# Kernel optimization log

Hardware: AMD Instinct MI355X
Metric: run time of the kernel (lower is better)

Reference implementation:

```python
import jax, jax.numpy as jnp
import numpy as np

TEMPERATURE = 1.0
WEIGHT = 1.0


def _transitivity_sum(rel):
    """rel: [N, N] relation probabilities for one (batch, relation) slice.
    Computes sum_{a,b,c} relu(rel[a,b] - rel[a,c] * rel[b,c]) via a scan over c
    (outer product of column c), keeping memory at O(N^2) instead of O(N^3)."""
    def step(acc, col):  # col = rel[:, c], shape [N]
        viol = jax.nn.relu(rel - col[:, None] * col[None, :])  # [N, N]
        return acc + jnp.sum(viol), None
    acc, _ = jax.lax.scan(step, jnp.zeros((), rel.dtype), rel.T)
    return acc


def setup_inputs() -> dict:
    key = jax.random.key(0)
    B, N, R = 2, 512, 4
    relation_logits = jax.random.normal(key, (B, N, N, R), dtype=jnp.float32)
    entity_masks = jnp.ones((B, N), dtype=jnp.int32)
    return {"relation_logits": relation_logits, "entity_masks": entity_masks}


def reference(relation_logits, entity_masks):
    B, N, _, R = relation_logits.shape
    probs = jax.nn.sigmoid(relation_logits / TEMPERATURE)  # [B, N, N, R]
    m = (entity_masks > 0).astype(probs.dtype)             # [B, N]
    rel = probs * m[:, :, None, None] * m[:, None, :, None]
    # flatten (batch, relation) and vmap the per-matrix cubic reduction
    rel_br = jnp.transpose(rel, (0, 3, 1, 2)).reshape(B * R, N, N)
    per = jax.vmap(_transitivity_sum)(rel_br)              # [B*R]
    # per-batch loss = sum_r / R; final = weight * mean over batch
    return WEIGHT * jnp.sum(per) / (R * B)
```

## Files before the change

kernel.cpp:

```cpp
#include <hip/hip_runtime.h>
#include <math.h>

#define N      512
#define RNUM   4
#define BNUM   2
#define NSLICE (RNUM * BNUM)
#define TILE   128
#define CT     32
#define LSTR   136
#define CSPLIT 8
#define NCOLB  16
#define SCALE  0.0625f

typedef _Float16 half2_t __attribute__((ext_vector_type(2)));

__device__ __forceinline__ unsigned int h2u(half2_t h) {
  return __builtin_bit_cast(unsigned int, h);
}
__device__ __forceinline__ half2_t u2h(unsigned int u) {
  return __builtin_bit_cast(half2_t, u);
}

__device__ __forceinline__ float sigmoidf_(float x) {
  return 1.0f / (1.0f + __expf(-x));
}

__global__ void zero_out_kernel(float* out) { out[0] = 0.0f; }

__global__ __launch_bounds__(256) void prep_f16_kernel(const float* __restrict__ logits,
                                                       const int* __restrict__ masks,
                                                       _Float16* __restrict__ P,
                                                       float* __restrict__ out) {
  if (blockIdx.x == 0 && threadIdx.x == 0) out[0] = 0.0f;
  int t = blockIdx.x * 256 + threadIdx.x;
  int b = t >> 18;
  int rem = t & (N * N - 1);
  int i = rem >> 9;
  int j = rem & (N - 1);
  float4 lg = *(const float4*)(logits + (size_t)t * 4);
  float mm = ((masks[b * N + i] > 0) && (masks[b * N + j] > 0)) ? 1.0f : 0.0f;
  size_t base = (size_t)b * RNUM * N * N + rem;
  P[base + 0 * (size_t)N * N] = (_Float16)(mm * sigmoidf_(lg.x));
  P[base + 1 * (size_t)N * N] = (_Float16)(mm * sigmoidf_(lg.y));
  P[base + 2 * (size_t)N * N] = (_Float16)(mm * sigmoidf_(lg.z));
  P[base + 3 * (size_t)N * N] = (_Float16)(mm * sigmoidf_(lg.w));
}

__global__ __launch_bounds__(256) void work_f16_kernel(const _Float16* __restrict__ P,
                                                       float* __restrict__ out) {
  __shared__ _Float16 tA[CT][LSTR];
  __shared__ _Float16 tB[CT][LSTR];
  __shared__ float wsum[4];

  const int tid = threadIdx.x;
  const int bid = blockIdx.x;

  if (bid < NCOLB) {
    const int s    = bid >> 1;
    const int half = bid & 1;
    const int c    = half * 256 + tid;
    const _Float16* col = P + (size_t)s * N * N + c;
    float sum = 0.0f;
#pragma unroll 8
    for (int a = 0; a < N; ++a) sum += (float)col[(size_t)a * N];
    float v = sum * ((float)N - sum);
    for (int off = 32; off > 0; off >>= 1) v += __shfl_down(v, off, 64);
    const int wid = tid >> 6;
    if ((tid & 63) == 0) wsum[wid] = v;
    __syncthreads();
    if (tid == 0)
      atomicAdd(out, (wsum[0] + wsum[1] + wsum[2] + wsum[3]) * SCALE);
    return;
  }

  const int m  = bid - NCOLB;
  const int bt = m & 3;
  const int at = (m >> 2) & 3;
  const int s  = (m >> 4) & 7;
  const int cz = m >> 7;
  const int a0 = at * TILE;
  const int b0 = bt * TILE;
  const int cbeg = cz * (N / CSPLIT);
  const int cend = cbeg + (N / CSPLIT);

  const int ta = tid & 15;
  const int tb = tid >> 4;

  const _Float16* Ph = P + (size_t)s * N * N;

  half2_t nrab2[8][4];
#pragma unroll
  for (int x = 0; x < 8; ++x) {
    int ga = a0 + ((x >> 2) << 6) + ta * 4 + (x & 3);
    uint2 u0 = *(const uint2*)(Ph + (size_t)ga * N + b0 + tb * 4);
    uint2 u1 = *(const uint2*)(Ph + (size_t)ga * N + b0 + 64 + tb * 4);
    nrab2[x][0] = u2h(u0.x ^ 0x80008000u);
    nrab2[x][1] = u2h(u0.y ^ 0x80008000u);
    nrab2[x][2] = u2h(u1.x ^ 0x80008000u);
    nrab2[x][3] = u2h(u1.y ^ 0x80008000u);
  }

  float acc[8];
#pragma unroll
  for (int x = 0; x < 8; ++x) acc[x] = 0.0f;

  const int sx   = tid & 127;
  const int sarr = tid >> 7;
  const _Float16* srow = Ph + (size_t)((sarr ? b0 : a0) + sx) * N;
  _Float16* dcol = sarr ? &tB[0][sx] : &tA[0][sx];

  for (int c0 = cbeg; c0 < cend; c0 += CT) {
    __syncthreads();
    {
      const uint4* src = (const uint4*)(srow + c0);
      uint4 q0 = src[0];
      uint4 q1 = src[1];
      uint4 q2 = src[2];
      uint4 q3 = src[3];
      unsigned int w[16] = {q0.x, q0.y, q0.z, q0.w, q1.x, q1.y, q1.z, q1.w,
                            q2.x, q2.y, q2.z, q2.w, q3.x, q3.y, q3.z, q3.w};
      union { unsigned int u32; _Float16 h[2]; } cv;
#pragma unroll
      for (int k = 0; k < 16; ++k) {
        cv.u32 = w[k];
        dcol[(size_t)(2 * k) * LSTR]     = cv.h[0];
        dcol[(size_t)(2 * k + 1) * LSTR] = cv.h[1];
      }
    }
    __syncthreads();

    half2_t acc2[8][4];
#pragma unroll
    for (int x = 0; x < 8; ++x)
#pragma unroll
      for (int yp = 0; yp < 4; ++yp)
        acc2[x][yp] = u2h(0u);

#pragma unroll 4
    for (int c = 0; c < CT; ++c) {
      uint2 ua0 = *(const uint2*)&tA[c][ta * 4];
      uint2 ua1 = *(const uint2*)&tA[c][64 + ta * 4];
      uint2 ub0 = *(const uint2*)&tB[c][tb * 4];
      uint2 ub1 = *(const uint2*)&tB[c][64 + tb * 4];
      half2_t av[4] = {u2h(ua0.x), u2h(ua0.y), u2h(ua1.x), u2h(ua1.y)};
      half2_t bv[4] = {u2h(ub0.x), u2h(ub0.y), u2h(ub1.x), u2h(ub1.y)};
#pragma unroll
      for (int x = 0; x < 8; ++x) {
        _Float16 as = (x & 1) ? av[x >> 1].y : av[x >> 1].x;
        half2_t asp = {as, as};
#pragma unroll
        for (int yp = 0; yp < 4; ++yp) {
          half2_t t2 = __builtin_elementwise_fma(asp, bv[yp], nrab2[x][yp]);
          acc2[x][yp] += u2h(h2u(t2) & 0x7FFF7FFFu);
        }
      }
    }

#pragma unroll
    for (int x = 0; x < 8; ++x) {
      float fx = acc[x];
#pragma unroll
      for (int yp = 0; yp < 4; ++yp)
        fx += (float)acc2[x][yp].x + (float)acc2[x][yp].y;
      acc[x] = fx;
    }
  }

  float tsum = 0.0f;
#pragma unroll
  for (int x = 0; x < 8; ++x) tsum += acc[x];

  for (int off = 32; off > 0; off >>= 1) tsum += __shfl_down(tsum, off, 64);

  const int wid = tid >> 6;
  if ((tid & 63) == 0) wsum[wid] = tsum;
  __syncthreads();
  if (tid == 0)
    atomicAdd(out, (wsum[0] + wsum[1] + wsum[2] + wsum[3]) * SCALE);
}

#define FCT    64
#define FSTR   132
#define FCSPL  4

__global__ __launch_bounds__(256, 2) void work_f32_fallback(const float* __restrict__ logits,
                                                            const int* __restrict__ masks,
                                                            float* __restrict__ out) {
  __shared__ __align__(16) float tA[FCT][FSTR];
  __shared__ __align__(16) float tB[FCT][FSTR];
  __shared__ float wsum[4];

  const int tid = threadIdx.x;
  const int bid = blockIdx.x;

  if (bid < NCOLB) {
    const int s    = bid >> 1;
    const int half = bid & 1;
    const int c    = half * 256 + tid;
    const int bb   = s >> 2;
    const int r    = s & 3;
    const int* mrow = masks + bb * N;
    float mc = (mrow[c] > 0) ? 1.0f : 0.0f;
    float sum = 0.0f;
#pragma unroll 4
    for (int a = 0; a < N; ++a) {
      float ma = (mrow[a] > 0) ? 1.0f : 0.0f;
      size_t idx = ((size_t)(bb * N + a) * N + c) * RNUM + r;
      sum += sigmoidf_(logits[idx]) * ma * mc;
    }
    float v = sum * ((float)N - sum);
    for (int off = 32; off > 0; off >>= 1) v += __shfl_down(v, off, 64);
    const int wid = tid >> 6;
    if ((tid & 63) == 0) wsum[wid] = v;
    __syncthreads();
    if (tid == 0)
      atomicAdd(out, (wsum[0] + wsum[1] + wsum[2] + wsum[3]) * SCALE);
    return;
  }

  const int m  = bid - NCOLB;
  const int bt = m & 3;
  const int at = (m >> 2) & 3;
  const int s  = (m >> 4) & 7;
  const int cz = m >> 7;
  const int a0 = at * TILE;
  const int b0 = bt * TILE;
  const int bb = s >> 2;
  const int r  = s & 3;
  const int cbeg = cz * (N / FCSPL);
  const int cend = cbeg + (N / FCSPL);

  const int ta = tid & 15;
  const int tb = tid >> 4;
  const int* mrow = masks + bb * N;

  float rab[8][8];
#pragma unroll
  for (int x = 0; x < 8; ++x) {
    int ra = a0 + ((x >> 2) << 6) + ta * 4 + (x & 3);
    float ma = (mrow[ra] > 0) ? 1.0f : 0.0f;
#pragma unroll
    for (int y = 0; y < 8; ++y) {
      int cb = b0 + ((y >> 2) << 6) + tb * 4 + (y & 3);
      float mb = (mrow[cb] > 0) ? 1.0f : 0.0f;
      size_t idx = ((size_t)(bb * N + ra) * N + cb) * RNUM + r;
      rab[x][y] = sigmoidf_(logits[idx]) * ma * mb;
    }
  }

  float acc[8][2];
#pragma unroll
  for (int x = 0; x < 8; ++x) { acc[x][0] = 0.0f; acc[x][1] = 0.0f; }

  for (int c0 = cbeg; c0 < cend; c0 += FCT) {
    __syncthreads();
#pragma unroll
    for (int it = 0; it < 32; ++it) {
      int e = it * 256 + tid;
      int c = e & 63;
      int i = e >> 6;
      int pc = ((((i >> 2) ^ ((c >> 2) & 31)) & 31) << 2) | (i & 3);
      float mc = (mrow[c0 + c] > 0) ? 1.0f : 0.0f;
      {
        float mi = (mrow[a0 + i] > 0) ? 1.0f : 0.0f;
        size_t idx = ((size_t)(bb * N + a0 + i) * N + (c0 + c)) * RNUM + r;
        tA[c][pc] = sigmoidf_(logits[idx]) * mi * mc;
      }
      {
        float mi = (mrow[b0 + i] > 0) ? 1.0f : 0.0f;
        size_t idx = ((size_t)(bb * N + b0 + i) * N + (c0 + c)) * RNUM + r;
        tB[c][pc] = sigmoidf_(logits[idx]) * mi * mc;
      }
    }
    __syncthreads();

#pragma unroll 2
    for (int cg = 0; cg < FCT / 4; ++cg) {
      const float* pa = &tA[cg * 4][((ta ^ cg) & 31) << 2];
      const float* pb = &tB[cg * 4][((tb ^ cg) & 31) << 2];
#pragma unroll
      for (int dc = 0; dc < 4; ++dc) {
        float4 a0v = *(const float4*)(pa + dc * FSTR);
        float4 a1v = *(const float4*)(pa + dc * FSTR + 64);
        float4 b0v = *(const float4*)(pb + dc * FSTR);
        float4 b1v = *(const float4*)(pb + dc * FSTR + 64);
        float avv[8] = {a0v.x, a0v.y, a0v.z, a0v.w, a1v.x, a1v.y, a1v.z, a1v.w};
        float bvv[8] = {b0v.x, b0v.y, b0v.z, b0v.w, b1v.x, b1v.y, b1v.z, b1v.w};
#pragma unroll
        for (int x = 0; x < 8; ++x) {
#pragma unroll
          for (int y = 0; y < 4; ++y)
            acc[x][0] += fabsf(fmaf(-avv[x], bvv[y], rab[x][y]));
#pragma unroll
          for (int y = 4; y < 8; ++y)
            acc[x][1] += fabsf(fmaf(-avv[x], bvv[y], rab[x][y]));
        }
      }
    }
  }

  float tsum = 0.0f;
#pragma unroll
  for (int x = 0; x < 8; ++x) tsum += acc[x][0] + acc[x][1];
  for (int off = 32; off > 0; off >>= 1) tsum += __shfl_down(tsum, off, 64);
  const int wid = tid >> 6;
  if ((tid & 63) == 0) wsum[wid] = tsum;
  __syncthreads();
  if (tid == 0)
    atomicAdd(out, (wsum[0] + wsum[1] + wsum[2] + wsum[3]) * SCALE);
}

extern "C" void kernel_launch(void* const* d_in, const int* in_sizes, int n_in,
                              void* d_out, int out_size, void* d_ws, size_t ws_size,
                              hipStream_t stream) {
  const float* logits = (const float*)d_in[0];
  const int*   masks  = (const int*)d_in[1];
  float*       out    = (float*)d_out;

  const size_t P_BYTES = (size_t)NSLICE * N * N * sizeof(_Float16);

  if (ws_size >= P_BYTES) {
    _Float16* P = (_Float16*)d_ws;
    prep_f16_kernel<<<(BNUM * N * N) / 256, 256, 0, stream>>>(logits, masks, P, out);
    const int nblocks = NCOLB + 4 * 4 * NSLICE * CSPLIT;
    work_f16_kernel<<<nblocks, 256, 0, stream>>>(P, out);
  } else {
    zero_out_kernel<<<1, 1, 0, stream>>>(out);
    const int nblocks = NCOLB + 4 * 4 * NSLICE * FCSPL;
    work_f32_fallback<<<nblocks, 256, 0, stream>>>(logits, masks, out);
  }
}
```

Before: 124.2 us.

## Swizzle LDS tiles along c and vectorize packed-half FMA over c

The f16 work kernel now stages a single 64-wide c-chunk into row-major LDS tiles with an XOR swizzle. It reads 8 halves per 128-bit LDS load and packs two c values per half2 FMA, with rab broadcast into both lanes. This removes the per-element scalar broadcast of a, the per-32-c float flush and the column-scatter LDS stores. The kernel also adds a launch-bounds occupancy hint, and the sigmoid uses a hardware reciprocal. In exchange, half-precision accumulators now sum more terms before conversion to float, which may lose accuracy.

```diff
diff --git a/kernel.cpp b/kernel.cpp
--- a/kernel.cpp
+++ b/kernel.cpp
@@ -6,8 +6,7 @@
 #define BNUM   2
 #define NSLICE (RNUM * BNUM)
 #define TILE   128
-#define CT     32
-#define LSTR   136
+#define CT     64
 #define CSPLIT 8
 #define NCOLB  16
 #define SCALE  0.0625f
@@ -22,7 +21,7 @@
 }
 
 __device__ __forceinline__ float sigmoidf_(float x) {
-  return 1.0f / (1.0f + __expf(-x));
+  return __builtin_amdgcn_rcpf(1.0f + __expf(-x));
 }
 
 __global__ void zero_out_kernel(float* out) { out[0] = 0.0f; }
@@ -46,10 +45,10 @@
   P[base + 3 * (size_t)N * N] = (_Float16)(mm * sigmoidf_(lg.w));
 }
 
-__global__ __launch_bounds__(256) void work_f16_kernel(const _Float16* __restrict__ P,
-                                                       float* __restrict__ out) {
-  __shared__ _Float16 tA[CT][LSTR];
-  __shared__ _Float16 tB[CT][LSTR];
+__global__ __launch_bounds__(256, 2) void work_f16_kernel(const _Float16* __restrict__ P,
+                                                          float* __restrict__ out) {
+  __shared__ __align__(16) _Float16 tA[128 * CT];
+  __shared__ __align__(16) _Float16 tB[128 * CT];
   __shared__ float wsum[4];
 
   const int tid = threadIdx.x;
@@ -80,95 +79,89 @@
   const int cz = m >> 7;
   const int a0 = at * TILE;
   const int b0 = bt * TILE;
-  const int cbeg = cz * (N / CSPLIT);
-  const int cend = cbeg + (N / CSPLIT);
+  const int c0 = cz * CT;
 
   const int ta = tid & 15;
   const int tb = tid >> 4;
 
   const _Float16* Ph = P + (size_t)s * N * N;
 
-  half2_t nrab2[8][4];
+  half2_t bc[8][8];
 #pragma unroll
   for (int x = 0; x < 8; ++x) {
-    int ga = a0 + ((x >> 2) << 6) + ta * 4 + (x & 3);
-    uint2 u0 = *(const uint2*)(Ph + (size_t)ga * N + b0 + tb * 4);
-    uint2 u1 = *(const uint2*)(Ph + (size_t)ga * N + b0 + 64 + tb * 4);
-    nrab2[x][0] = u2h(u0.x ^ 0x80008000u);
-    nrab2[x][1] = u2h(u0.y ^ 0x80008000u);
-    nrab2[x][2] = u2h(u1.x ^ 0x80008000u);
-    nrab2[x][3] = u2h(u1.y ^ 0x80008000u);
-  }
-
-  float acc[8];
-#pragma unroll
-  for (int x = 0; x < 8; ++x) acc[x] = 0.0f;
-
-  const int sx   = tid & 127;
-  const int sarr = tid >> 7;
-  const _Float16* srow = Ph + (size_t)((sarr ? b0 : a0) + sx) * N;
-  _Float16* dcol = sarr ? &tB[0][sx] : &tA[0][sx];
-
-  for (int c0 = cbeg; c0 < cend; c0 += CT) {
-    __syncthreads();
-    {
-      const uint4* src = (const uint4*)(srow + c0);
-      uint4 q0 = src[0];
-      uint4 q1 = src[1];
-      uint4 q2 = src[2];
-      uint4 q3 = src[3];
-      unsigned int w[16] = {q0.x, q0.y, q0.z, q0.w, q1.x, q1.y, q1.z, q1.w,
-                            q2.x, q2.y, q2.z, q2.w, q3.x, q3.y, q3.z, q3.w};
-      union { unsigned int u32; _Float16 h[2]; } cv;
-#pragma unroll
-      for (int k = 0; k < 16; ++k) {
-        cv.u32 = w[k];
-        dcol[(size_t)(2 * k) * LSTR]     = cv.h[0];
-        dcol[(size_t)(2 * k + 1) * LSTR] = cv.h[1];
-      }
-    }
-    __syncthreads();
-
-    half2_t acc2[8][4];
-#pragma unroll
-    for (int x = 0; x < 8; ++x)
-#pragma unroll
-      for (int yp = 0; yp < 4; ++yp)
-        acc2[x][yp] = u2h(0u);
-
-#pragma unroll 4
-    for (int c = 0; c < CT; ++c) {
-      uint2 ua0 = *(const uint2*)&tA[c][ta * 4];
-      uint2 ua1 = *(const uint2*)&tA[c][64 + ta * 4];
-      uint2 ub0 = *(const uint2*)&tB[c][tb * 4];
-      uint2 ub1 = *(const uint2*)&tB[c][64 + tb * 4];
-      half2_t av[4] = {u2h(ua0.x), u2h(ua0.y), u2h(ua1.x), u2h(ua1.y)};
-      half2_t bv[4] = {u2h(ub0.x), u2h(ub0.y), u2h(ub1.x), u2h(ub1.y)};
-#pragma unroll
-      for (int x = 0; x < 8; ++x) {
-        _Float16 as = (x & 1) ? av[x >> 1].y : av[x >> 1].x;
-        half2_t asp = {as, as};
-#pragma unroll
-        for (int yp = 0; yp < 4; ++yp) {
-          half2_t t2 = __builtin_elementwise_fma(asp, bv[yp], nrab2[x][yp]);
-          acc2[x][yp] += u2h(h2u(t2) & 0x7FFF7FFFu);
+    int ga = a0 + ((x >> 2) << 6) + (ta << 2) + (x & 3);
+    const _Float16* rrow = Ph + (size_t)ga * N + b0;
+    uint2 u0 = *(const uint2*)(rrow + (tb << 2));
+    uint2 u1 = *(const uint2*)(rrow + 64 + (tb << 2));
+    half2_t p0 = u2h(u0.x), p1 = u2h(u0.y), p2 = u2h(u1.x), p3 = u2h(u1.y);
+    bc[x][0] = half2_t{p0.x, p0.x};
+    bc[x][1] = half2_t{p0.y, p0.y};
+    bc[x][2] = half2_t{p1.x, p1.x};
+    bc[x][3] = half2_t{p1.y, p1.y};
+    bc[x][4] = half2_t{p2.x, p2.x};
+    bc[x][5] = half2_t{p2.y, p2.y};
+    bc[x][6] = half2_t{p3.x, p3.x};
+    bc[x][7] = half2_t{p3.y, p3.y};
+  }
+
+  {
+    const int sx   = tid & 127;
+    const int sarr = tid >> 7;
+    const _Float16* srow = Ph + (size_t)((sarr ? b0 : a0) + sx) * N + c0;
+    _Float16* dst = (sarr ? tB : tA) + sx * CT;
+    const int key = (sx >> 2) & 7;
+    const uint4* src = (const uint4*)srow;
+#pragma unroll
+    for (int cbg = 0; cbg < 8; ++cbg) {
+      uint4 q = src[cbg];
+      *(uint4*)&dst[(cbg ^ key) << 3] = q;
+    }
+  }
+  __syncthreads();
+
+  half2_t acc2[8][2];
+#pragma unroll
+  for (int x = 0; x < 8; ++x) { acc2[x][0] = u2h(0u); acc2[x][1] = u2h(0u); }
+
+  const int keyA = ta & 7;
+  const int keyB = tb & 7;
+  int arow[8], brow[8];
+#pragma unroll
+  for (int x = 0; x < 8; ++x)
+    arow[x] = (((x >> 2) << 6) | (ta << 2) | (x & 3)) * CT;
+#pragma unroll
+  for (int y = 0; y < 8; ++y)
+    brow[y] = (((y >> 2) << 6) | (tb << 2) | (y & 3)) * CT;
+
+#pragma unroll 1
+  for (int cb = 0; cb < 8; ++cb) {
+    uint4 bq[8];
+#pragma unroll
+    for (int y = 0; y < 8; ++y)
+      bq[y] = *(const uint4*)&tB[brow[y] + ((cb ^ keyB) << 3)];
+#pragma unroll
+    for (int x = 0; x < 8; ++x) {
+      uint4 aq = *(const uint4*)&tA[arow[x] + ((cb ^ keyA) << 3)];
+      unsigned int au[4] = {aq.x, aq.y, aq.z, aq.w};
+#pragma unroll
+      for (int y = 0; y < 8; ++y) {
+        unsigned int bu[4] = {bq[y].x, bq[y].y, bq[y].z, bq[y].w};
+#pragma unroll
+        for (int k = 0; k < 4; ++k) {
+          half2_t t2 = __builtin_elementwise_fma(-u2h(au[k]), u2h(bu[k]),
+                                                 bc[x][y]);
+          acc2[x][y & 1] += u2h(h2u(t2) & 0x7FFF7FFFu);
         }
       }
     }
-
-#pragma unroll
-    for (int x = 0; x < 8; ++x) {
-      float fx = acc[x];
-#pragma unroll
-      for (int yp = 0; yp < 4; ++yp)
-        fx += (float)acc2[x][yp].x + (float)acc2[x][yp].y;
-      acc[x] = fx;
-    }
   }
 
   float tsum = 0.0f;
 #pragma unroll
-  for (int x = 0; x < 8; ++x) tsum += acc[x];
+  for (int x = 0; x < 8; ++x) {
+    tsum += (float)acc2[x][0].x + (float)acc2[x][0].y +
+            (float)acc2[x][1].x + (float)acc2[x][1].y;
+  }
 
   for (int off = 32; off > 0; off >>= 1) tsum += __shfl_down(tsum, off, 64);
 
@@ -186,8 +179,8 @@
 __global__ __launch_bounds__(256, 2) void work_f32_fallback(const float* __restrict__ logits,
                                                             const int* __restrict__ masks,
                                                             float* __restrict__ out) {
-  __shared__ __align__(16) float tA[FCT][FSTR];
-  __shared__ __align__(16) float tB[FCT][FSTR];
+  __shared__ __align__(16) float tAf[FCT][FSTR];
+  __shared__ __align__(16) float tBf[FCT][FSTR];
   __shared__ float wsum[4];
 
   const int tid = threadIdx.x;
@@ -264,20 +257,20 @@
       {
         float mi = (mrow[a0 + i] > 0) ? 1.0f : 0.0f;
         size_t idx = ((size_t)(bb * N + a0 + i) * N + (c0 + c)) * RNUM + r;
-        tA[c][pc] = sigmoidf_(logits[idx]) * mi * mc;
+        tAf[c][pc] = sigmoidf_(logits[idx]) * mi * mc;
       }
       {
         float mi = (mrow[b0 + i] > 0) ? 1.0f : 0.0f;
         size_t idx = ((size_t)(bb * N + b0 + i) * N + (c0 + c)) * RNUM + r;
-        tB[c][pc] = sigmoidf_(logits[idx]) * mi * mc;
+        tBf[c][pc] = sigmoidf_(logits[idx]) * mi * mc;
       }
     }
     __syncthreads();
 
 #pragma unroll 2
     for (int cg = 0; cg < FCT / 4; ++cg) {
-      const float* pa = &tA[cg * 4][((ta ^ cg) & 31) << 2];
-      const float* pb = &tB[cg * 4][((tb ^ cg) & 31) << 2];
+      const float* pa = &tAf[cg * 4][((ta ^ cg) & 31) << 2];
+      const float* pb = &tBf[cg * 4][((tb ^ cg) & 31) << 2];
 #pragma unroll
       for (int dc = 0; dc < 4; ++dc) {
         float4 a0v = *(const float4*)(pa + dc * FSTR);
```

Result: faster. 117.4 us (-5.5%).
